# Kernel tuning notes

Hardware: AMD Instinct MI355X
Metric: run time of the kernel (lower is better)

The kernel has to match this reference:

```python
import jax, jax.numpy as jnp
import numpy as np

N, D, E, R = 1024, 128, 32768, 32  # nodes, hidden, edges, rank-net width
EPS = 1e-5


def setup_inputs() -> dict:
    key = jax.random.key(0)
    ks = jax.random.split(key, 16)
    s = 0.02
    f32 = jnp.float32
    return {
        "x": jax.random.normal(ks[0], (N, D), f32),
        "edge_index": jax.random.randint(ks[1], (2, E), 0, N),
        # SAGEConv (mean aggr): lin_l (with bias) on aggregated neighbors, lin_r (no bias) on root
        "W_l": jax.random.normal(ks[2], (D, D), f32) * s,
        "b_l": jnp.zeros((D,), f32),
        "W_r": jax.random.normal(ks[3], (D, D), f32) * s,
        # rank_net: Linear(D,32) -> ReLU -> Linear(32,1)
        "W1": jax.random.normal(ks[4], (R, D), f32) * s,
        "b1": jnp.zeros((R,), f32),
        "W2": jax.random.normal(ks[5], (1, R), f32) * s,
        "b2": jnp.zeros((1,), f32),
        # MambaBlock params
        "Wp": jax.random.normal(ks[6], (4 * D, D), f32) * s,   # proj, no bias
        "A": jax.random.normal(ks[7], (1, 1, D), f32) * s,
        "Bp": jax.random.normal(ks[8], (1, D, 1), f32) * s,
        "Dp": jnp.ones((1,), f32),
        "Wd": jax.random.normal(ks[9], (D, D), f32) * s,       # delta linear
        "bd": jnp.zeros((D,), f32),
    }


def reference(x, edge_index, W_l, b_l, W_r, W1, b1, W2, b2, Wp, A, Bp, Dp, Wd, bd):
    src, dst = edge_index[0], edge_index[1]

    # ---- SAGEConv (mean) + residual + GELU ----
    agg = jax.ops.segment_sum(x[src], dst, num_segments=N)                      # [N,D]
    cnt = jax.ops.segment_sum(jnp.ones((E,), x.dtype), dst, num_segments=N)    # [N]
    mean = agg / jnp.maximum(cnt, 1.0)[:, None]
    x_gnn = mean @ W_l.T + b_l + x @ W_r.T + x
    x_gnn = jax.nn.gelu(x_gnn, approximate=False)

    # ---- dynamic sort: rank_net score + degree, argsort descending ----
    scores = (jax.nn.relu(x_gnn @ W1.T + b1) @ W2.T + b2)[:, 0]                # [N]
    deg = jnp.zeros((N,), x.dtype).at[src].add(1.0).at[dst].add(1.0)
    scores = scores + deg
    idx = jnp.argsort(-scores)          # soft_rank is monotone -> same ordering as raw scores
    xs = x_gnn[idx]                      # [N,D]

    # ---- MambaBlock on the sorted node sequence (batch=1, seq_len=N, hidden=D) ----
    proj = xs @ Wp.T                                    # [N,4D]
    delta, _Bs, Cs, residual = jnp.split(proj, 4, axis=-1)  # split B is unused (as in source)
    delta = jax.nn.softplus(delta @ Wd.T + bd)          # [N,D]
    Av = A[0, 0]                                        # [D]
    Bv = Bp[0, :, 0]                                    # [D]
    dA = (jnp.exp(delta * Av) * Bv).T                   # [D,N]  einsum('blh,bhn->bhl') with n=1
    dB = jnp.cumsum(delta * Bv, axis=0).T               # [D,N]  cumsum over seq, n=1
    u = xs.T                                            # [D,N]
    Ct = Cs.T                                           # [D,N]
    kernel = jnp.einsum('hl,hn->hnl', dA, u) + dB[:, None, :]   # [D,N,N] large intermediate
    y = jnp.einsum('hnl,hn->hl', kernel, Ct).T                  # [N,D]
    out = y + residual * Dp[0]

    # F.layer_norm without affine params
    mu = out.mean(-1, keepdims=True)
    var = out.var(-1, keepdims=True)
    out = (out - mu) / jnp.sqrt(var + EPS)

    inv = jnp.argsort(idx)
    return x + out[inv]
```

## Files before the change

### kernel.cpp

```cpp
#include <hip/hip_runtime.h>

namespace {
constexpr int N   = 1024;
constexpr int D   = 128;
constexpr int E   = 32768;
constexpr int CAP = 128;

using short8  = __attribute__((ext_vector_type(8))) short;
using floatx4 = __attribute__((ext_vector_type(4))) float;

__device__ __forceinline__ unsigned short f2bf(float f){
  unsigned int u = __float_as_uint(f);
  unsigned int r = (u + 0x7FFFu + ((u >> 16) & 1u)) >> 16;
  return (unsigned short)r;
}
__device__ __forceinline__ float bf2f(unsigned short b){
  return __uint_as_float(((unsigned int)b) << 16);
}
__device__ __forceinline__ short8 ldfrag(const float* p){
  float4 a = *(const float4*)p;
  float4 b = *(const float4*)(p + 4);
  short8 r;
  r[0]=(short)f2bf(a.x); r[1]=(short)f2bf(a.y); r[2]=(short)f2bf(a.z); r[3]=(short)f2bf(a.w);
  r[4]=(short)f2bf(b.x); r[5]=(short)f2bf(b.y); r[6]=(short)f2bf(b.z); r[7]=(short)f2bf(b.w);
  return r;
}

__global__ __launch_bounds__(256) void k_zero(
    int* __restrict__ cnt, int* __restrict__ srcdeg,
    const float* __restrict__ Wl, const float* __restrict__ Wr,
    const float* __restrict__ Wd, const float* __restrict__ W1,
    const float* __restrict__ Wp,
    unsigned short* __restrict__ wlb, unsigned short* __restrict__ wrb,
    unsigned short* __restrict__ wdb, unsigned short* __restrict__ w1b,
    unsigned short* __restrict__ wpb)
{
  int t = threadIdx.x, b = blockIdx.x;
  if(b == 0){
    ((int4*)cnt)[t]    = make_int4(0,0,0,0);
    ((int4*)srcdeg)[t] = make_int4(0,0,0,0);
    return;
  }
  const int T = 16384*3 + 4096 + 65536;
  int stride = 128*256;
  for(int i = (b-1)*256 + t; i < T; i += stride){
    float v; unsigned short* dst;
    if(i < 16384){            v = Wl[i];          dst = &wlb[i]; }
    else if(i < 32768){       v = Wr[i-16384];    dst = &wrb[i-16384]; }
    else if(i < 49152){       v = Wd[i-32768];    dst = &wdb[i-32768]; }
    else if(i < 53248){       v = W1[i-49152];    dst = &w1b[i-49152]; }
    else {                    v = Wp[i-53248];    dst = &wpb[i-53248]; }
    *dst = f2bf(v);
  }
}

__global__ void k_edges(const int* __restrict__ ei, int* __restrict__ cnt,
                        int* __restrict__ srcdeg, int* __restrict__ bucket){
  int e = blockIdx.x*256 + threadIdx.x;
  if(e < E){
    int s = ei[e], d = ei[E+e];
    int slot = atomicAdd(&cnt[d], 1);
    if(slot < CAP) bucket[d*CAP + slot] = s;
    atomicAdd(&srcdeg[s], 1);
  }
}

__global__ __launch_bounds__(512) void k_mean(const float* __restrict__ x,
    const int* __restrict__ cnt, const int* __restrict__ bucket,
    float* __restrict__ mean, float* __restrict__ s1, float* __restrict__ s2){
  __shared__ float sacc[3][128];
  int t = threadIdx.x;
  int n = blockIdx.x;
  if(n == 0 && t < D){ s1[t] = 0.f; s2[t] = 0.f; }
  int f = t & 127, j2 = t >> 7;
  int c0 = cnt[n];
  int c = c0 < CAP ? c0 : CAP;
  const int* bk = bucket + n*CAP;
  int ch = (c + 3) >> 2;
  int beg = j2 * ch, end = beg + ch < c ? beg + ch : c;
  float a0=0.f, a1=0.f, a2=0.f, a3=0.f;
  int j = beg;
  for(; j+3 < end; j += 4){
    int i0=bk[j], i1=bk[j+1], i2=bk[j+2], i3=bk[j+3];
    a0 += x[i0*D+f]; a1 += x[i1*D+f]; a2 += x[i2*D+f]; a3 += x[i3*D+f];
  }
  for(; j < end; ++j) a0 += x[bk[j]*D+f];
  float part = (a0+a1)+(a2+a3);
  if(j2 > 0) sacc[j2-1][f] = part;
  __syncthreads();
  if(j2 == 0){
    float tot = part + sacc[0][f] + sacc[1][f] + sacc[2][f];
    mean[n*D + f] = tot / (float)(c0 > 1 ? c0 : 1);
  }
}


__global__ __launch_bounds__(64) void k_g1(
    const float* __restrict__ x, const float* __restrict__ mean,
    const unsigned short* __restrict__ wlb, const float* __restrict__ bl,
    const unsigned short* __restrict__ wrb, unsigned short* __restrict__ xg)
{
  int bid = blockIdx.x;
  int strip = bid >> 3, ct = bid & 7;
  int l = threadIdx.x, lr = l & 15, lg = l >> 4;
  int r0 = strip*16;

  const float* mrow = mean + (size_t)(r0+lr)*D + lg*8;
  const float* xrow = x    + (size_t)(r0+lr)*D + lg*8;
  short8 am[4], ax[4];
  #pragma unroll
  for(int s = 0; s < 4; ++s){ am[s] = ldfrag(mrow + s*32); ax[s] = ldfrag(xrow + s*32); }

  const unsigned short* wl = wlb + (size_t)(ct*16+lr)*D + lg*8;
  const unsigned short* wr = wrb + (size_t)(ct*16+lr)*D + lg*8;
  floatx4 acc = {0.f,0.f,0.f,0.f};
  #pragma unroll
  for(int s = 0; s < 4; ++s) acc = __builtin_amdgcn_mfma_f32_16x16x32_bf16(am[s], *(const short8*)(wl + s*32), acc, 0,0,0);
  #pragma unroll
  for(int s = 0; s < 4; ++s) acc = __builtin_amdgcn_mfma_f32_16x16x32_bf16(ax[s], *(const short8*)(wr + s*32), acc, 0,0,0);

  int col = ct*16 + lr;
  float blv = bl[col];
  #pragma unroll
  for(int rg = 0; rg < 4; ++rg){
    int row = lg*4 + rg;
    float v = acc[rg] + blv + x[(size_t)(r0+row)*D + col];
    float g = 0.5f*v*(1.0f + erff(v*0.7071067811865475f));
    xg[(size_t)(r0+row)*D + col] = f2bf(g);
  }
}

__global__ __launch_bounds__(64) void k_g2(
    const unsigned short* __restrict__ xg,
    const unsigned short* __restrict__ wpb, const unsigned short* __restrict__ w1b,
    const float* __restrict__ b1, const float* __restrict__ W2,
    const float* __restrict__ b2,
    const int* __restrict__ cnt, const int* __restrict__ srcdeg,
    unsigned short* __restrict__ dr, float* __restrict__ res,
    float* __restrict__ s1, float* __restrict__ s2,
    float* __restrict__ scores)
{
  int bid = blockIdx.x;
  int strip = bid / 25, tt = bid - strip*25;
  int l = threadIdx.x, lr = l & 15, lg = l >> 4;
  int r0 = strip*16;

  const unsigned short* agp = xg + (size_t)(r0+lr)*D + lg*8;
  short8 ag[4];
  #pragma unroll
  for(int s = 0; s < 4; ++s) ag[s] = *(const short8*)(agp + s*32);

  if(tt < 24){
    int seg = tt >> 3, ctl = tt & 7;
    int wrow = (seg == 0) ? ctl*16 : (seg == 1) ? (2*D + ctl*16) : (3*D + ctl*16);
    const unsigned short* bp = wpb + (size_t)(wrow + lr)*D + lg*8;
    floatx4 acc = {0.f,0.f,0.f,0.f};
    #pragma unroll
    for(int s = 0; s < 4; ++s) acc = __builtin_amdgcn_mfma_f32_16x16x32_bf16(ag[s], *(const short8*)(bp + s*32), acc, 0,0,0);
    if(seg == 0){
      int col = ctl*16 + lr;
      #pragma unroll
      for(int rg = 0; rg < 4; ++rg) dr[(size_t)(r0+lg*4+rg)*D + col] = f2bf(acc[rg]);
    } else if(seg == 1){
      int h = ctl*16 + lr;
      float ls1 = 0.f, ls2 = 0.f;
      #pragma unroll
      for(int rg = 0; rg < 4; ++rg){
        float c = acc[rg];
        ls1 += bf2f(xg[(size_t)(r0+lg*4+rg)*D + h]) * c;
        ls2 += c;
      }
      ls1 += __shfl_xor(ls1, 16); ls1 += __shfl_xor(ls1, 32);
      ls2 += __shfl_xor(ls2, 16); ls2 += __shfl_xor(ls2, 32);
      if(lg == 0){ atomicAdd(&s1[h], ls1); atomicAdd(&s2[h], ls2); }
    } else {
      int col = ctl*16 + lr;
      #pragma unroll
      for(int rg = 0; rg < 4; ++rg) res[(size_t)(r0+lg*4+rg)*D + col] = acc[rg];
    }
  } else {
    floatx4 sa0 = {0.f,0.f,0.f,0.f}, sa1 = {0.f,0.f,0.f,0.f};
    const unsigned short* w10 = w1b + (size_t)(lr)*D + lg*8;
    const unsigned short* w11 = w1b + (size_t)(16+lr)*D + lg*8;
    #pragma unroll
    for(int s = 0; s < 4; ++s){
      sa0 = __builtin_amdgcn_mfma_f32_16x16x32_bf16(ag[s], *(const short8*)(w10 + s*32), sa0, 0,0,0);
      sa1 = __builtin_amdgcn_mfma_f32_16x16x32_bf16(ag[s], *(const short8*)(w11 + s*32), sa1, 0,0,0);
    }
    float b10 = b1[lr], b11 = b1[16+lr];
    float w20 = W2[lr], w21 = W2[16+lr];
    #pragma unroll
    for(int rg = 0; rg < 4; ++rg){
      float v = fmaxf(sa0[rg] + b10, 0.f)*w20 + fmaxf(sa1[rg] + b11, 0.f)*w21;
      v += __shfl_xor(v, 1); v += __shfl_xor(v, 2);
      v += __shfl_xor(v, 4); v += __shfl_xor(v, 8);
      if(lr == 0){
        int row = r0 + lg*4 + rg;
        scores[row] = v + b2[0] + (float)(cnt[row] + srcdeg[row]);
      }
    }
  }
}

__global__ __launch_bounds__(64) void k_g3rank(
    const unsigned short* __restrict__ dr,
    const unsigned short* __restrict__ wdb, const float* __restrict__ bd,
    float* __restrict__ delta,
    const float* __restrict__ scores, int* __restrict__ sidx)
{
  int bid = blockIdx.x;
  int l = threadIdx.x;
  if(bid < 512){
    int strip = bid >> 3, ct = bid & 7;
    int lr = l & 15, lg = l >> 4;
    int r0 = strip*16;
    const unsigned short* adp = dr + (size_t)(r0+lr)*D + lg*8;
    short8 ad[4];
    #pragma unroll
    for(int s = 0; s < 4; ++s) ad[s] = *(const short8*)(adp + s*32);
    const unsigned short* wd = wdb + (size_t)(ct*16+lr)*D + lg*8;
    floatx4 acc = {0.f,0.f,0.f,0.f};
    #pragma unroll
    for(int s = 0; s < 4; ++s) acc = __builtin_amdgcn_mfma_f32_16x16x32_bf16(ad[s], *(const short8*)(wd + s*32), acc, 0,0,0);
    int col = ct*16 + lr;
    float bdv = bd[col];
    #pragma unroll
    for(int rg = 0; rg < 4; ++rg){
      float d2 = acc[rg] + bdv;
      float sp = (d2 > 20.f) ? d2 : log1pf(expf(d2));
      delta[(size_t)(r0+lg*4+rg)*D + col] = sp;
    }
  } else {
    int i = bid - 512;
    float si = scores[i];
    int c = 0;
    #pragma unroll
    for(int ch = 0; ch < 4; ++ch){
      float4 sj = *(const float4*)&scores[l*4 + ch*256];
      #pragma unroll
      for(int k = 0; k < 4; ++k){
        int j = l*4 + ch*256 + k;
        float s = (k==0)?sj.x:(k==1)?sj.y:(k==2)?sj.z:sj.w;
        c += (s > si || (s == si && j < i)) ? 1 : 0;
      }
    }
    #pragma unroll
    for(int m = 1; m < 64; m <<= 1) c += __shfl_xor(c, m);
    if(l == 0) sidx[c] = i;
  }
}

__global__ __launch_bounds__(1024) void k_cumsum(const float* __restrict__ delta,
     const int* __restrict__ sidx, const float* __restrict__ Bp, float* __restrict__ pfx){
  int t = threadIdx.x, h = blockIdx.x;
  int i = sidx[t];
  float v = delta[(size_t)i*D + h] * Bp[h];
  int lane = t & 63, w = t >> 6;
  #pragma unroll
  for(int o2 = 1; o2 < 64; o2 <<= 1){
    float nb = __shfl_up(v, o2, 64);
    if(lane >= o2) v += nb;
  }
  __shared__ float wsum[16];
  if(lane == 63) wsum[w] = v;
  __syncthreads();
  float pref = 0.f;
  #pragma unroll
  for(int i2 = 0; i2 < 16; ++i2){
    float s = wsum[i2];
    if(i2 < w) pref += s;
  }
  pfx[(size_t)t*D + h] = v + pref;
}

__global__ __launch_bounds__(128) void k_final(
    const float* __restrict__ delta, const float* __restrict__ res,
    const float* __restrict__ pfx, const int* __restrict__ sidx,
    const float* __restrict__ s1, const float* __restrict__ s2,
    const float* __restrict__ A, const float* __restrict__ Bp,
    const float* __restrict__ Dp, const float* __restrict__ x,
    float* __restrict__ out){
  int l = blockIdx.x, h = threadIdx.x;
  int i = sidx[l];
  float dlt = delta[i*D + h];
  float dAv = expf(dlt * A[h]) * Bp[h];
  float o = dAv * s1[h] + pfx[l*D + h] * s2[h] + res[i*D + h] * Dp[0];
  __shared__ float sm1[2], sm2[2];
  float v = o;
  v += __shfl_down(v, 32); v += __shfl_down(v, 16); v += __shfl_down(v, 8);
  v += __shfl_down(v, 4);  v += __shfl_down(v, 2);  v += __shfl_down(v, 1);
  int wid = h >> 6, lane = h & 63;
  if(lane == 0) sm1[wid] = v;
  __syncthreads();
  float mean = (sm1[0] + sm1[1]) * (1.0f/(float)D);
  float cdev = o - mean;
  float cv = cdev * cdev;
  cv += __shfl_down(cv, 32); cv += __shfl_down(cv, 16); cv += __shfl_down(cv, 8);
  cv += __shfl_down(cv, 4);  cv += __shfl_down(cv, 2);  cv += __shfl_down(cv, 1);
  if(lane == 0) sm2[wid] = cv;
  __syncthreads();
  float var = (sm2[0] + sm2[1]) * (1.0f/(float)D);
  float nrm = cdev * rsqrtf(var + 1e-5f);
  out[i*D + h] = x[i*D + h] + nrm;
}

}

extern "C" void kernel_launch(void* const* d_in, const int* in_sizes, int n_in,
                              void* d_out, int out_size, void* d_ws, size_t ws_size,
                              hipStream_t stream){
  const float* x   = (const float*)d_in[0];
  const int*   ei  = (const int*)d_in[1];
  const float* Wl  = (const float*)d_in[2];
  const float* bl  = (const float*)d_in[3];
  const float* Wr  = (const float*)d_in[4];
  const float* W1  = (const float*)d_in[5];
  const float* b1  = (const float*)d_in[6];
  const float* W2  = (const float*)d_in[7];
  const float* b2  = (const float*)d_in[8];
  const float* Wp  = (const float*)d_in[9];
  const float* A   = (const float*)d_in[10];
  const float* Bp  = (const float*)d_in[11];
  const float* Dp  = (const float*)d_in[12];
  const float* Wd  = (const float*)d_in[13];
  const float* bd  = (const float*)d_in[14];

  char* ws = (char*)d_ws;
  size_t o = 0;
  auto alloc = [&](size_t bytes)->char*{
    char* p = ws + o;
    o = (o + bytes + 255) & ~(size_t)255;
    return p;
  };
  float* s1     = (float*)alloc(D*4);
  float* s2     = (float*)alloc(D*4);
  int*   cnt    = (int*)  alloc(N*4);
  int*   srcdeg = (int*)  alloc(N*4);
  int*   bucket = (int*)  alloc((size_t)N*CAP*4);
  float* meanb  = (float*)alloc((size_t)N*D*4);
  unsigned short* xg  = (unsigned short*)alloc((size_t)N*D*2);
  unsigned short* dr  = (unsigned short*)alloc((size_t)N*D*2);
  unsigned short* wlb = (unsigned short*)alloc((size_t)D*D*2);
  unsigned short* wrb = (unsigned short*)alloc((size_t)D*D*2);
  unsigned short* wdb = (unsigned short*)alloc((size_t)D*D*2);
  unsigned short* w1b = (unsigned short*)alloc((size_t)32*D*2);
  unsigned short* wpb = (unsigned short*)alloc((size_t)4*D*D*2);
  float* scores = (float*)alloc(N*4);
  int*   sidx   = (int*)  alloc(N*4);
  float* delta  = (float*)alloc((size_t)N*D*4);
  float* res    = (float*)alloc((size_t)N*D*4);
  float* pfx    = (float*)alloc((size_t)N*D*4);
  (void)ws_size; (void)in_sizes; (void)n_in; (void)out_size;

  k_zero  <<<129, 256, 0, stream>>>(cnt, srcdeg, Wl, Wr, Wd, W1, Wp, wlb, wrb, wdb, w1b, wpb);
  k_edges <<<(E+255)/256, 256, 0, stream>>>(ei, cnt, srcdeg, bucket);
  k_mean  <<<N, 512, 0, stream>>>(x, cnt, bucket, meanb, s1, s2);
  k_g1    <<<64*8, 64, 0, stream>>>(x, meanb, wlb, bl, wrb, xg);
  k_g2    <<<64*25, 64, 0, stream>>>(xg, wpb, w1b, b1, W2, b2, cnt, srcdeg, dr, res, s1, s2, scores);
  k_g3rank<<<512+1024, 64, 0, stream>>>(dr, wdb, bd, delta, scores, sidx);
  k_cumsum<<<D, 1024, 0, stream>>>(delta, sidx, Bp, pfx);
  k_final <<<N, 128, 0, stream>>>(delta, res, pfx, sidx, s1, s2, A, Bp, Dp, x, (float*)d_out);
}
```

Measured before the change: 48.99 us.

## Fuse SAGE GEMM into projection kernel via LDS tile, pack two rows per final block

Merges k_g1 into k_g2. Each block now recomputes its 16-row GELU(SAGE) strip in shared memory and no longer reads xg from global memory, which drops one launch and the xg round trip. The price is redundant work: each strip's 16x128 SAGE GEMM is recomputed by all 25 blocks of that strip rather than once. Separately, k_final now handles two rows per 256-thread block, halving its block count.

```diff
diff --git a/kernel.cpp b/kernel.cpp
--- a/kernel.cpp
+++ b/kernel.cpp
@@ -95,43 +95,10 @@
 }
 
 
-__global__ __launch_bounds__(64) void k_g1(
+__global__ __launch_bounds__(64) void k_g12(
     const float* __restrict__ x, const float* __restrict__ mean,
     const unsigned short* __restrict__ wlb, const float* __restrict__ bl,
-    const unsigned short* __restrict__ wrb, unsigned short* __restrict__ xg)
-{
-  int bid = blockIdx.x;
-  int strip = bid >> 3, ct = bid & 7;
-  int l = threadIdx.x, lr = l & 15, lg = l >> 4;
-  int r0 = strip*16;
-
-  const float* mrow = mean + (size_t)(r0+lr)*D + lg*8;
-  const float* xrow = x    + (size_t)(r0+lr)*D + lg*8;
-  short8 am[4], ax[4];
-  #pragma unroll
-  for(int s = 0; s < 4; ++s){ am[s] = ldfrag(mrow + s*32); ax[s] = ldfrag(xrow + s*32); }
-
-  const unsigned short* wl = wlb + (size_t)(ct*16+lr)*D + lg*8;
-  const unsigned short* wr = wrb + (size_t)(ct*16+lr)*D + lg*8;
-  floatx4 acc = {0.f,0.f,0.f,0.f};
-  #pragma unroll
-  for(int s = 0; s < 4; ++s) acc = __builtin_amdgcn_mfma_f32_16x16x32_bf16(am[s], *(const short8*)(wl + s*32), acc, 0,0,0);
-  #pragma unroll
-  for(int s = 0; s < 4; ++s) acc = __builtin_amdgcn_mfma_f32_16x16x32_bf16(ax[s], *(const short8*)(wr + s*32), acc, 0,0,0);
-
-  int col = ct*16 + lr;
-  float blv = bl[col];
-  #pragma unroll
-  for(int rg = 0; rg < 4; ++rg){
-    int row = lg*4 + rg;
-    float v = acc[rg] + blv + x[(size_t)(r0+row)*D + col];
-    float g = 0.5f*v*(1.0f + erff(v*0.7071067811865475f));
-    xg[(size_t)(r0+row)*D + col] = f2bf(g);
-  }
-}
-
-__global__ __launch_bounds__(64) void k_g2(
-    const unsigned short* __restrict__ xg,
+    const unsigned short* __restrict__ wrb,
     const unsigned short* __restrict__ wpb, const unsigned short* __restrict__ w1b,
     const float* __restrict__ b1, const float* __restrict__ W2,
     const float* __restrict__ b2,
@@ -140,15 +107,41 @@
     float* __restrict__ s1, float* __restrict__ s2,
     float* __restrict__ scores)
 {
+  __shared__ unsigned short sxg[16][136];
   int bid = blockIdx.x;
   int strip = bid / 25, tt = bid - strip*25;
   int l = threadIdx.x, lr = l & 15, lg = l >> 4;
   int r0 = strip*16;
 
-  const unsigned short* agp = xg + (size_t)(r0+lr)*D + lg*8;
+  short8 am[4], ax[4];
+  const float* mrow = mean + (size_t)(r0+lr)*D + lg*8;
+  const float* xrow = x    + (size_t)(r0+lr)*D + lg*8;
+  #pragma unroll
+  for(int s = 0; s < 4; ++s){ am[s] = ldfrag(mrow + s*32); ax[s] = ldfrag(xrow + s*32); }
+  #pragma unroll
+  for(int ct = 0; ct < 8; ++ct){
+    const unsigned short* wl = wlb + (size_t)(ct*16+lr)*D + lg*8;
+    const unsigned short* wr = wrb + (size_t)(ct*16+lr)*D + lg*8;
+    floatx4 acc = {0.f,0.f,0.f,0.f};
+    #pragma unroll
+    for(int s = 0; s < 4; ++s) acc = __builtin_amdgcn_mfma_f32_16x16x32_bf16(am[s], *(const short8*)(wl + s*32), acc, 0,0,0);
+    #pragma unroll
+    for(int s = 0; s < 4; ++s) acc = __builtin_amdgcn_mfma_f32_16x16x32_bf16(ax[s], *(const short8*)(wr + s*32), acc, 0,0,0);
+    int col = ct*16 + lr;
+    float blv = bl[col];
+    #pragma unroll
+    for(int rg = 0; rg < 4; ++rg){
+      int row = lg*4 + rg;
+      float v = acc[rg] + blv + x[(size_t)(r0+row)*D + col];
+      float g = 0.5f*v*(1.0f + erff(v*0.7071067811865475f));
+      sxg[row][col] = f2bf(g);
+    }
+  }
+  __syncthreads();
+
   short8 ag[4];
   #pragma unroll
-  for(int s = 0; s < 4; ++s) ag[s] = *(const short8*)(agp + s*32);
+  for(int s = 0; s < 4; ++s) ag[s] = *(const short8*)&sxg[lr][s*32 + lg*8];
 
   if(tt < 24){
     int seg = tt >> 3, ctl = tt & 7;
@@ -167,7 +160,7 @@
       #pragma unroll
       for(int rg = 0; rg < 4; ++rg){
         float c = acc[rg];
-        ls1 += bf2f(xg[(size_t)(r0+lg*4+rg)*D + h]) * c;
+        ls1 += bf2f(sxg[lg*4+rg][h]) * c;
         ls2 += c;
       }
       ls1 += __shfl_xor(ls1, 16); ls1 += __shfl_xor(ls1, 32);
@@ -273,35 +266,36 @@
   pfx[(size_t)t*D + h] = v + pref;
 }
 
-__global__ __launch_bounds__(128) void k_final(
+__global__ __launch_bounds__(256) void k_final(
     const float* __restrict__ delta, const float* __restrict__ res,
     const float* __restrict__ pfx, const int* __restrict__ sidx,
     const float* __restrict__ s1, const float* __restrict__ s2,
     const float* __restrict__ A, const float* __restrict__ Bp,
     const float* __restrict__ Dp, const float* __restrict__ x,
     float* __restrict__ out){
-  int l = blockIdx.x, h = threadIdx.x;
+  int b = blockIdx.x, t = threadIdx.x;
+  int half = t >> 7, hh = t & 127;
+  int l = b*2 + half;
   int i = sidx[l];
-  float dlt = delta[i*D + h];
-  float dAv = expf(dlt * A[h]) * Bp[h];
-  float o = dAv * s1[h] + pfx[l*D + h] * s2[h] + res[i*D + h] * Dp[0];
-  __shared__ float sm1[2], sm2[2];
+  float dlt = delta[(size_t)i*D + hh];
+  float dAv = expf(dlt * A[hh]) * Bp[hh];
+  float o = dAv * s1[hh] + pfx[(size_t)l*D + hh] * s2[hh] + res[(size_t)i*D + hh] * Dp[0];
+  __shared__ float fm[2][2], fv[2][2];
   float v = o;
   v += __shfl_down(v, 32); v += __shfl_down(v, 16); v += __shfl_down(v, 8);
   v += __shfl_down(v, 4);  v += __shfl_down(v, 2);  v += __shfl_down(v, 1);
-  int wid = h >> 6, lane = h & 63;
-  if(lane == 0) sm1[wid] = v;
-  __syncthreads();
-  float mean = (sm1[0] + sm1[1]) * (1.0f/(float)D);
-  float cdev = o - mean;
-  float cv = cdev * cdev;
+  int wid = (t >> 6) & 1;
+  if((t & 63) == 0) fm[half][wid] = v;
+  __syncthreads();
+  float mean = (fm[half][0] + fm[half][1]) * (1.0f/128.0f);
+  float cd = o - mean;
+  float cv = cd*cd;
   cv += __shfl_down(cv, 32); cv += __shfl_down(cv, 16); cv += __shfl_down(cv, 8);
   cv += __shfl_down(cv, 4);  cv += __shfl_down(cv, 2);  cv += __shfl_down(cv, 1);
-  if(lane == 0) sm2[wid] = cv;
-  __syncthreads();
-  float var = (sm2[0] + sm2[1]) * (1.0f/(float)D);
-  float nrm = cdev * rsqrtf(var + 1e-5f);
-  out[i*D + h] = x[i*D + h] + nrm;
+  if((t & 63) == 0) fv[half][wid] = cv;
+  __syncthreads();
+  float var = (fv[half][0] + fv[half][1]) * (1.0f/128.0f);
+  out[(size_t)i*D + hh] = x[(size_t)i*D + hh] + cd * rsqrtf(var + 1e-5f);
 }
 
 }
@@ -338,7 +332,6 @@
   int*   srcdeg = (int*)  alloc(N*4);
   int*   bucket = (int*)  alloc((size_t)N*CAP*4);
   float* meanb  = (float*)alloc((size_t)N*D*4);
-  unsigned short* xg  = (unsigned short*)alloc((size_t)N*D*2);
   unsigned short* dr  = (unsigned short*)alloc((size_t)N*D*2);
   unsigned short* wlb = (unsigned short*)alloc((size_t)D*D*2);
   unsigned short* wrb = (unsigned short*)alloc((size_t)D*D*2);
@@ -355,9 +348,9 @@
   k_zero  <<<129, 256, 0, stream>>>(cnt, srcdeg, Wl, Wr, Wd, W1, Wp, wlb, wrb, wdb, w1b, wpb);
   k_edges <<<(E+255)/256, 256, 0, stream>>>(ei, cnt, srcdeg, bucket);
   k_mean  <<<N, 512, 0, stream>>>(x, cnt, bucket, meanb, s1, s2);
-  k_g1    <<<64*8, 64, 0, stream>>>(x, meanb, wlb, bl, wrb, xg);
-  k_g2    <<<64*25, 64, 0, stream>>>(xg, wpb, w1b, b1, W2, b2, cnt, srcdeg, dr, res, s1, s2, scores);
+  k_g12   <<<64*25, 64, 0, stream>>>(x, meanb, wlb, bl, wrb, wpb, w1b, b1, W2, b2,
+                                     cnt, srcdeg, dr, res, s1, s2, scores);
   k_g3rank<<<512+1024, 64, 0, stream>>>(dr, wdb, bd, delta, scores, sidx);
   k_cumsum<<<D, 1024, 0, stream>>>(delta, sidx, Bp, pfx);
-  k_final <<<N, 128, 0, stream>>>(delta, res, pfx, sidx, s1, s2, A, Bp, Dp, x, (float*)d_out);
-}
+  k_final <<<N/2, 256, 0, stream>>>(delta, res, pfx, sidx, s1, s2, A, Bp, Dp, x, (float*)d_out);
+}
```

Measured after the change: 60.71 us. 1.24x slower.
